# Optimization experiments

Measured on AMD Instinct MI355X. Metric: run time of the kernel, lower is better.

## Reference

```python
import jax, jax.numpy as jnp
import numpy as np

B, T, DIM, H, HD, K = 4, 2048, 1024, 16, 64, 4
QK = H * HD          # 1024
VD = 2 * H * HD      # 2048
EPS = 1e-5


def zrms(x, g):
    # zero-centered RMS norm with learned scale
    x = x - jnp.mean(x, axis=-1, keepdims=True)
    return x * jax.lax.rsqrt(jnp.mean(x * x, axis=-1, keepdims=True) + EPS) * g


def causal_dwconv(x, w):
    # x: [B,T,C], w: [K,1,C] (keras depthwise Conv1D kernel, groups=C)
    k = w.shape[0]
    return jax.lax.conv_general_dilated(
        x, w, window_strides=(1,), padding=[(k - 1, 0)],
        dimension_numbers=('NWC', 'WIO', 'NWC'),
        feature_group_count=x.shape[-1])


def setup_inputs() -> dict:
    key = jax.random.key(0)
    ks = jax.random.split(key, 12)
    s = lambda *sh: 1.0 / np.sqrt(sh[0])
    return {
        'x':  jax.random.normal(ks[0], (B, T, DIM), jnp.float32),
        'Wq': jax.random.normal(ks[1], (DIM, QK), jnp.float32) * s(DIM),
        'Wk': jax.random.normal(ks[2], (DIM, QK), jnp.float32) * s(DIM),
        'Wv': jax.random.normal(ks[3], (DIM, VD), jnp.float32) * s(DIM),
        'gq': jnp.ones((QK,), jnp.float32),
        'gk': jnp.ones((QK,), jnp.float32),
        'gv': jnp.ones((VD,), jnp.float32),
        'cq': jax.random.normal(ks[4], (K, 1, QK), jnp.float32) * 0.5,
        'ck': jax.random.normal(ks[5], (K, 1, QK), jnp.float32) * 0.5,
        'cv': jax.random.normal(ks[6], (K, 1, VD), jnp.float32) * 0.5,
        'Wa': jax.random.normal(ks[7], (DIM, H), jnp.float32) * s(DIM),
        'Wb': jax.random.normal(ks[8], (DIM, H), jnp.float32) * s(DIM),
        'Wo': jax.random.normal(ks[9], (VD, DIM), jnp.float32) * s(VD),
        'Wg': jax.random.normal(ks[10], (DIM, DIM), jnp.float32) * s(DIM),
    }


def reference(x, Wq, Wk, Wv, gq, gk, gv, cq, ck, cv, Wa, Wb, Wo, Wg):
    # 1) projections  2) zero-centered RMSNorm  3) causal depthwise conv (+silu)
    q = jax.nn.silu(causal_dwconv(zrms(x @ Wq, gq), cq))   # [B,T,QK]
    k = jax.nn.silu(causal_dwconv(zrms(x @ Wk, gk), ck))   # [B,T,QK]
    v = jax.nn.silu(causal_dwconv(zrms(x @ Wv, gv), cv))   # [B,T,VD]

    q = q.reshape(B, T, H, HD)
    k = k.reshape(B, T, H, HD)
    v = v.reshape(B, T, H, 2 * HD)

    # 4) per-head gating params
    alpha = jax.nn.sigmoid(x @ Wa)  # [B,T,H]
    beta = jax.nn.sigmoid(x @ Wb)   # [B,T,H]

    # 5) gated delta-rule recurrence over time (state S: [B,H,2*HD,HD])
    def step(S, inp):
        qt, kt, vt, at, bt = inp  # [B,H,HD],[B,H,HD],[B,H,2HD],[B,H],[B,H]
        a = at[..., None, None]
        upd = S + bt[..., None, None] * jnp.einsum('bhv,bhk->bhvk', vt, kt)
        S = a * upd + (1.0 - a) * S
        o = jnp.einsum('bhvk,bhk->bhv', S, qt)  # Q_t readout
        return S, o

    S0 = jnp.zeros((B, H, 2 * HD, HD), x.dtype)
    xs = (q.transpose(1, 0, 2, 3), k.transpose(1, 0, 2, 3),
          v.transpose(1, 0, 2, 3), alpha.transpose(1, 0, 2),
          beta.transpose(1, 0, 2))
    _, o = jax.lax.scan(step, S0, xs)          # o: [T,B,H,2HD]
    o = o.transpose(1, 0, 2, 3).reshape(B, T, VD)

    # 6) output projection + sigmoid output gate
    proj = o @ Wo                              # [B,T,DIM]
    return jax.nn.sigmoid(proj @ Wg) * proj
```

## Files before the change

kernel.cpp:

```cpp
#include <hip/hip_runtime.h>
#include <hip/hip_bf16.h>
#include <math.h>

#define RTOT 8192
#define TSEQ 2048

typedef __attribute__((ext_vector_type(8))) short short8;
typedef __attribute__((ext_vector_type(4))) float f32x4;
typedef unsigned short u16;
typedef unsigned int u32;

union U16x8 { uint4 v; u16 s[8]; };

__device__ __forceinline__ float sigmoidf_(float x) { return 1.f / (1.f + expf(-x)); }
__device__ __forceinline__ float bf2f(u16 v) { u32 u = ((u32)v) << 16; float f; __builtin_memcpy(&f, &u, 4); return f; }
__device__ __forceinline__ u16 f2bf(float f) {
  u32 u; __builtin_memcpy(&u, &f, 4);
  u32 r = (u + 0x7FFFu + ((u >> 16) & 1u)) >> 16;
  return (u16)r;
}
__device__ __forceinline__ void split2(float x, u16& h, u16& l) {
  u16 hh = f2bf(x);
  float hf = bf2f(hh);
  h = hh; l = f2bf(x - hf);
}

typedef const void __attribute__((address_space(1))) gvoid_t;
typedef void __attribute__((address_space(3))) lvoid_t;
__device__ __forceinline__ void gload_lds16(const void* g, void* l) {
  __builtin_amdgcn_global_load_lds((gvoid_t*)g, (lvoid_t*)l, 16, 0, 0);
}

__device__ __forceinline__ void xcd_remap(int& bx, int& by) {
  int gx = gridDim.x, nwg = gx * gridDim.y;
  int bid = blockIdx.y * gx + blockIdx.x;
  int cpx = nwg >> 3;
  int swz = (bid & 7) * cpx + (bid >> 3);
  bx = swz % gx; by = swz / gx;
}

__global__ __launch_bounds__(512) void gemm_sp_big(const u16* __restrict__ Ah, const u16* __restrict__ Al,
                                                   const u16* __restrict__ Bh, const u16* __restrict__ Bl,
                                                   float* __restrict__ Cf,
                                                   int M, int N, int K) {
  __shared__ u16 lds[2][4][256 * 32];
  int bx, by; xcd_remap(bx, by);
  const int tid = threadIdx.x;
  const int l = tid & 63, w = tid >> 6;
  const int wr = w >> 2, wc = w & 3;
  const int m0 = by * 256, n0 = bx * 256;
  const int fr = l & 15, fq = l >> 4;
  const int koff = 8 * (fq ^ (fr & 3));
  const int srow = tid >> 2;
  const int scol = ((tid & 3) ^ (srow & 3)) * 8;
  const u16* gA_h = Ah + (size_t)(m0 + srow) * K + scol;
  const u16* gA_l = Al + (size_t)(m0 + srow) * K + scol;
  const u16* gB_h = Bh + (size_t)(n0 + srow) * K + scol;
  const u16* gB_l = Bl + (size_t)(n0 + srow) * K + scol;
  const int lo = srow * 32 + (tid & 3) * 8;
  const int NT = K >> 5;

#define STG(buf, mat, src, t)                                 \
  do {                                                        \
    const int k0_ = (t) << 5;                                 \
    gload_lds16(src + k0_, &lds[buf][mat][lo]);               \
    gload_lds16(src + 128 * K + k0_, &lds[buf][mat][lo + 4096]); \
  } while (0)

#define MFMA_PAIR(mi, a_h, a_l)                                                        \
  do {                                                                                 \
    _Pragma("unroll")                                                                  \
    for (int n = 0; n < 4; ++n) {                                                      \
      acc[mi][n] = __builtin_amdgcn_mfma_f32_16x16x32_bf16(a_h, bh8[n], acc[mi][n], 0, 0, 0); \
      acc[mi][n] = __builtin_amdgcn_mfma_f32_16x16x32_bf16(a_h, bl8[n], acc[mi][n], 0, 0, 0); \
      acc[mi][n] = __builtin_amdgcn_mfma_f32_16x16x32_bf16(a_l, bh8[n], acc[mi][n], 0, 0, 0); \
    }                                                                                  \
  } while (0)

  f32x4 acc[8][4] = {};
  STG(0, 0, gA_h, 0); STG(0, 1, gA_l, 0); STG(0, 2, gB_h, 0); STG(0, 3, gB_l, 0);
  asm volatile("s_waitcnt vmcnt(0)" ::: "memory");
  __builtin_amdgcn_s_barrier();

  for (int t = 0; t < NT; ++t) {
    const int c = t & 1, o = c ^ 1;
    const bool pf = (t + 1 < NT);
    short8 bh8[4], bl8[4];
    {
#pragma unroll
      for (int n = 0; n < 4; ++n) {
        bh8[n] = *(const short8*)&lds[c][2][(wc * 64 + n * 16 + fr) * 32 + koff];
        bl8[n] = *(const short8*)&lds[c][3][(wc * 64 + n * 16 + fr) * 32 + koff];
      }
      short8 a0h = *(const short8*)&lds[c][0][(wr * 128 + 0 * 16 + fr) * 32 + koff];
      short8 a1h = *(const short8*)&lds[c][0][(wr * 128 + 1 * 16 + fr) * 32 + koff];
      short8 a0l = *(const short8*)&lds[c][1][(wr * 128 + 0 * 16 + fr) * 32 + koff];
      short8 a1l = *(const short8*)&lds[c][1][(wr * 128 + 1 * 16 + fr) * 32 + koff];
      if (pf) { STG(o, 2, gB_h, t + 1); STG(o, 3, gB_l, t + 1); }
      __builtin_amdgcn_s_barrier();
      asm volatile("s_waitcnt lgkmcnt(0)" ::: "memory");
      __builtin_amdgcn_s_setprio(1);
      MFMA_PAIR(0, a0h, a0l);
      MFMA_PAIR(1, a1h, a1l);
      __builtin_amdgcn_s_setprio(0);
      __builtin_amdgcn_s_barrier();
    }
    {
      short8 a0h = *(const short8*)&lds[c][0][(wr * 128 + 2 * 16 + fr) * 32 + koff];
      short8 a1h = *(const short8*)&lds[c][0][(wr * 128 + 3 * 16 + fr) * 32 + koff];
      short8 a0l = *(const short8*)&lds[c][1][(wr * 128 + 2 * 16 + fr) * 32 + koff];
      short8 a1l = *(const short8*)&lds[c][1][(wr * 128 + 3 * 16 + fr) * 32 + koff];
      if (pf) { STG(o, 0, gA_h, t + 1); STG(o, 1, gA_l, t + 1); }
      __builtin_amdgcn_s_barrier();
      asm volatile("s_waitcnt lgkmcnt(0)" ::: "memory");
      __builtin_amdgcn_s_setprio(1);
      MFMA_PAIR(2, a0h, a0l);
      MFMA_PAIR(3, a1h, a1l);
      __builtin_amdgcn_s_setprio(0);
      __builtin_amdgcn_s_barrier();
    }
    {
      short8 a0h = *(const short8*)&lds[c][0][(wr * 128 + 4 * 16 + fr) * 32 + koff];
      short8 a1h = *(const short8*)&lds[c][0][(wr * 128 + 5 * 16 + fr) * 32 + koff];
      short8 a0l = *(const short8*)&lds[c][1][(wr * 128 + 4 * 16 + fr) * 32 + koff];
      short8 a1l = *(const short8*)&lds[c][1][(wr * 128 + 5 * 16 + fr) * 32 + koff];
      __builtin_amdgcn_s_barrier();
      asm volatile("s_waitcnt lgkmcnt(0)" ::: "memory");
      __builtin_amdgcn_s_setprio(1);
      MFMA_PAIR(4, a0h, a0l);
      MFMA_PAIR(5, a1h, a1l);
      __builtin_amdgcn_s_setprio(0);
      __builtin_amdgcn_s_barrier();
    }
    {
      short8 a0h = *(const short8*)&lds[c][0][(wr * 128 + 6 * 16 + fr) * 32 + koff];
      short8 a1h = *(const short8*)&lds[c][0][(wr * 128 + 7 * 16 + fr) * 32 + koff];
      short8 a0l = *(const short8*)&lds[c][1][(wr * 128 + 6 * 16 + fr) * 32 + koff];
      short8 a1l = *(const short8*)&lds[c][1][(wr * 128 + 7 * 16 + fr) * 32 + koff];
      __builtin_amdgcn_s_barrier();
      asm volatile("s_waitcnt lgkmcnt(0)" ::: "memory");
      __builtin_amdgcn_s_setprio(1);
      MFMA_PAIR(6, a0h, a0l);
      MFMA_PAIR(7, a1h, a1l);
      __builtin_amdgcn_s_setprio(0);
      if (pf) asm volatile("s_waitcnt vmcnt(0)" ::: "memory");
      __builtin_amdgcn_s_barrier();
    }
  }
#undef STG
#undef MFMA_PAIR
#pragma unroll
  for (int m = 0; m < 8; ++m)
#pragma unroll
    for (int n = 0; n < 4; ++n)
#pragma unroll
      for (int r = 0; r < 4; ++r)
        Cf[(size_t)(m0 + wr * 128 + m * 16 + 4 * fq + r) * N + (n0 + wc * 64 + n * 16 + fr)] = acc[m][n][r];
}

template<int EPI>
__global__ __launch_bounds__(256) void gemm_sp(const u16* __restrict__ Ah, const u16* __restrict__ Al,
                                               const u16* __restrict__ Bh, const u16* __restrict__ Bl,
                                               float* __restrict__ Cf, u16* __restrict__ Ph,
                                               u16* __restrict__ Pl, const u16* __restrict__ Pinh,
                                               const u16* __restrict__ Pinl,
                                               int M, int N, int K) {
  __shared__ u16 Ash[128 * 32], Asl[128 * 32];
  __shared__ u16 Bsh[128 * 32], Bsl[128 * 32];
  int bx, by; xcd_remap(bx, by);
  const int tid = threadIdx.x;
  const int l = tid & 63, w = tid >> 6;
  const int m0 = by * 128, n0 = bx * 128;
  const int wr = w >> 1, wc = w & 1;
  f32x4 acc[4][4] = {};
  const int srow = (w << 5) + (l >> 2);
  const int scol = (l & 3) << 3;
  const size_t gA = (size_t)(m0 + srow) * K + scol;
  const size_t gB = (size_t)(n0 + srow) * K + scol;
  const int lo0 = (w * 2 + 0) * 512, lo1 = (w * 2 + 1) * 512;
  const int arow = wr * 64 + (l & 15), brow = wc * 64 + (l & 15);
  const int koff = 8 * (l >> 4);
  for (int k0 = 0; k0 < K; k0 += 32) {
    gload_lds16(Ah + gA + k0, &Ash[lo0]);
    gload_lds16(Ah + gA + 16 * K + k0, &Ash[lo1]);
    gload_lds16(Al + gA + k0, &Asl[lo0]);
    gload_lds16(Al + gA + 16 * K + k0, &Asl[lo1]);
    gload_lds16(Bh + gB + k0, &Bsh[lo0]);
    gload_lds16(Bh + gB + 16 * K + k0, &Bsh[lo1]);
    gload_lds16(Bl + gB + k0, &Bsl[lo0]);
    gload_lds16(Bl + gB + 16 * K + k0, &Bsl[lo1]);
    __syncthreads();
    short8 afh[4], afl[4], bfh[4], bfl[4];
#pragma unroll
    for (int m = 0; m < 4; ++m) {
      afh[m] = *(const short8*)&Ash[(arow + m * 16) * 32 + koff];
      afl[m] = *(const short8*)&Asl[(arow + m * 16) * 32 + koff];
    }
#pragma unroll
    for (int n = 0; n < 4; ++n) {
      bfh[n] = *(const short8*)&Bsh[(brow + n * 16) * 32 + koff];
      bfl[n] = *(const short8*)&Bsl[(brow + n * 16) * 32 + koff];
    }
#pragma unroll
    for (int m = 0; m < 4; ++m)
#pragma unroll
      for (int n = 0; n < 4; ++n) {
        acc[m][n] = __builtin_amdgcn_mfma_f32_16x16x32_bf16(afh[m], bfh[n], acc[m][n], 0, 0, 0);
        acc[m][n] = __builtin_amdgcn_mfma_f32_16x16x32_bf16(afh[m], bfl[n], acc[m][n], 0, 0, 0);
        acc[m][n] = __builtin_amdgcn_mfma_f32_16x16x32_bf16(afl[m], bfh[n], acc[m][n], 0, 0, 0);
      }
    __syncthreads();
  }
  const int rbase = m0 + wr * 64 + 4 * (l >> 4);
  const int cbase = n0 + wc * 64 + (l & 15);
#pragma unroll
  for (int m = 0; m < 4; ++m)
#pragma unroll
    for (int n = 0; n < 4; ++n)
#pragma unroll
      for (int r = 0; r < 4; ++r) {
        size_t idx = (size_t)(rbase + m * 16 + r) * N + (cbase + n * 16);
        float v = acc[m][n][r];
        if (EPI == 0) {
          Cf[idx] = v;
        } else if (EPI == 1) {
          u16 h, lo; split2(v, h, lo);
          Ph[idx] = h; Pl[idx] = lo;
        } else {
          float pin = bf2f(Pinh[idx]) + bf2f(Pinl[idx]);
          Cf[idx] = pin * sigmoidf_(v);
        }
      }
}

__global__ __launch_bounds__(256) void transcast_sp(const float* __restrict__ W,
                                                    u16* __restrict__ Wth, u16* __restrict__ Wtl,
                                                    int K, int N) {
  __shared__ float t[32][33];
  const int n0 = blockIdx.x * 32, k0 = blockIdx.y * 32;
  const int c = threadIdx.x & 31, rq = threadIdx.x >> 5;
#pragma unroll
  for (int i = 0; i < 4; ++i) t[rq * 4 + i][c] = W[(size_t)(k0 + rq * 4 + i) * N + n0 + c];
  __syncthreads();
#pragma unroll
  for (int i = 0; i < 4; ++i) {
    float v = t[c][rq * 4 + i];
    u16 h, lo; split2(v, h, lo);
    size_t idx = (size_t)(n0 + rq * 4 + i) * K + k0 + c;
    Wth[idx] = h; Wtl[idx] = lo;
  }
}

__global__ __launch_bounds__(256) void castx_sp(const float* __restrict__ x,
                                                u16* __restrict__ xh, u16* __restrict__ xl) {
  size_t i = (size_t)blockIdx.x * 256 + threadIdx.x;
  float4 v = ((const float4*)x)[i];
  ushort4 hh, ll;
  split2(v.x, hh.x, ll.x); split2(v.y, hh.y, ll.y);
  split2(v.z, hh.z, ll.z); split2(v.w, hh.w, ll.w);
  ((ushort4*)xh)[i] = hh; ((ushort4*)xl)[i] = ll;
}

template<int C, int GSCALE>
__global__ __launch_bounds__(C / 4) void conv_fs(const float* __restrict__ zn,
                                                 const float* __restrict__ w,
                                                 const float* __restrict__ g,
                                                 const float* __restrict__ gab,
                                                 u16* __restrict__ oh,
                                                 u16* __restrict__ ol) {
  constexpr int NW = C / 256;
  __shared__ float redA[NW * 4];
  __shared__ float redB[NW * 4];
  const int tid = threadIdx.x;
  const int row = blockIdx.x;
  const int t = row & (TSEQ - 1);
  const int c = tid * 4;
  const int lane = tid & 63, wid = tid >> 6;
  float4 xv[4];
  float psum[4];
#pragma unroll
  for (int d = 0; d < 4; ++d) {
    if (t - d >= 0) xv[d] = *(const float4*)(zn + (size_t)(row - d) * 4096 + c);
    else { xv[d].x = 0.f; xv[d].y = 0.f; xv[d].z = 0.f; xv[d].w = 0.f; }
    psum[d] = xv[d].x + xv[d].y + xv[d].z + xv[d].w;
  }
#pragma unroll
  for (int d = 0; d < 4; ++d)
#pragma unroll
    for (int o = 32; o > 0; o >>= 1) psum[d] += __shfl_xor(psum[d], o, 64);
  if (lane == 0) {
    redA[wid * 4 + 0] = psum[0]; redA[wid * 4 + 1] = psum[1];
    redA[wid * 4 + 2] = psum[2]; redA[wid * 4 + 3] = psum[3];
  }
  __syncthreads();
  float mean[4];
#pragma unroll
  for (int d = 0; d < 4; ++d) {
    float s = 0.f;
#pragma unroll
    for (int j = 0; j < NW; ++j) s += redA[j * 4 + d];
    mean[d] = s * (1.f / C);
  }
  float psq[4];
#pragma unroll
  for (int d = 0; d < 4; ++d) {
    float a = xv[d].x - mean[d], b = xv[d].y - mean[d];
    float e = xv[d].z - mean[d], f = xv[d].w - mean[d];
    psq[d] = a * a + b * b + e * e + f * f;
  }
#pragma unroll
  for (int d = 0; d < 4; ++d)
#pragma unroll
    for (int o = 32; o > 0; o >>= 1) psq[d] += __shfl_xor(psq[d], o, 64);
  if (lane == 0) {
    redB[wid * 4 + 0] = psq[0]; redB[wid * 4 + 1] = psq[1];
    redB[wid * 4 + 2] = psq[2]; redB[wid * 4 + 3] = psq[3];
  }
  __syncthreads();
  float rstd[4];
#pragma unroll
  for (int d = 0; d < 4; ++d) {
    float s = 0.f;
#pragma unroll
    for (int j = 0; j < NW; ++j) s += redB[j * 4 + d];
    rstd[d] = rsqrtf(s * (1.f / C) + 1e-5f);
  }
  float4 g4 = *(const float4*)(g + c);
  float4 acc; acc.x = 0.f; acc.y = 0.f; acc.z = 0.f; acc.w = 0.f;
#pragma unroll
  for (int d = 0; d < 4; ++d) {
    if (t - d >= 0) {
      float4 wv = *(const float4*)(w + (size_t)(3 - d) * C + c);
      acc.x = fmaf((xv[d].x - mean[d]) * rstd[d] * g4.x, wv.x, acc.x);
      acc.y = fmaf((xv[d].y - mean[d]) * rstd[d] * g4.y, wv.y, acc.y);
      acc.z = fmaf((xv[d].z - mean[d]) * rstd[d] * g4.z, wv.z, acc.z);
      acc.w = fmaf((xv[d].w - mean[d]) * rstd[d] * g4.w, wv.w, acc.w);
    }
  }
  float a0 = acc.x * sigmoidf_(acc.x);
  float a1 = acc.y * sigmoidf_(acc.y);
  float a2 = acc.z * sigmoidf_(acc.z);
  float a3 = acc.w * sigmoidf_(acc.w);
  if (GSCALE) {
    float gv = gab[(size_t)row * 16 + (c >> 7)];
    a0 *= gv; a1 *= gv; a2 *= gv; a3 *= gv;
  }
  ushort4 hh, ll;
  split2(a0, hh.x, ll.x); split2(a1, hh.y, ll.y);
  split2(a2, hh.z, ll.z); split2(a3, hh.w, ll.w);
  *(ushort4*)(oh + (size_t)row * C + c) = hh;
  *(ushort4*)(ol + (size_t)row * C + c) = ll;
}

__global__ __launch_bounds__(256) void gab_kernel(const float* __restrict__ x,
                                                  const float* __restrict__ Wa,
                                                  const float* __restrict__ Wb,
                                                  float* __restrict__ gout) {
  __shared__ float xs[1024];
  __shared__ float partial[256];
  const int tid = threadIdx.x;
  const size_t row = blockIdx.x;
  *(float4*)(&xs[tid*4]) = *(const float4*)(x + row*1024 + tid*4);
  __syncthreads();
  const int h = tid & 31;
  const int seg = tid >> 5;
  const float* W = (h < 16) ? Wa : Wb;
  const int col = h & 15;
  float s = 0.f;
  const int k0 = seg * 128;
  for (int k = 0; k < 128; ++k) s = fmaf(xs[k0 + k], W[(size_t)(k0 + k) * 16 + col], s);
  partial[tid] = s;
  __syncthreads();
  if (tid < 32) {
    float t2 = 0.f;
#pragma unroll
    for (int j = 0; j < 8; ++j) t2 += partial[j*32 + tid];
    partial[tid] = t2;
  }
  __syncthreads();
  if (tid < 16)
    gout[row*16 + tid] = sigmoidf_(partial[tid]) * sigmoidf_(partial[tid + 16]);
}

__global__ __launch_bounds__(256) void scan_kernel(const u16* __restrict__ kh,
                                                   const u16* __restrict__ kl,
                                                   const u16* __restrict__ vgh,
                                                   const u16* __restrict__ vgl,
                                                   u16* __restrict__ Sph,
                                                   u16* __restrict__ Spl) {
  __shared__ float Ks[64][36];
  __shared__ float Vs[64][36];
  const int tid = threadIdx.x;
  const int bid = blockIdx.x;
  const int kq = bid & 1, vq = (bid >> 1) & 3, h = (bid >> 3) & 15, b = bid >> 7;
  const size_t rb = (size_t)b * TSEQ;
  const int vd_t = tid >> 3, kd0 = (tid & 7) * 4;
  float S[4] = {};
  const int sr = tid >> 2;
  const int cc0 = (tid & 3) * 8;
  for (int c = 0; c < 32; ++c) {
    {
      size_t koffg = (rb + (size_t)c * 64 + sr) * 1024 + h * 64 + kq * 32 + cc0;
      U16x8 a0, b0;
      a0.v = *(const uint4*)(kh + koffg);
      b0.v = *(const uint4*)(kl + koffg);
#pragma unroll
      for (int j = 0; j < 8; ++j) Ks[sr][cc0 + j] = bf2f(a0.s[j]) + bf2f(b0.s[j]);
      size_t voffg = (rb + (size_t)c * 64 + sr) * 2048 + h * 128 + vq * 32 + cc0;
      U16x8 va, vb;
      va.v = *(const uint4*)(vgh + voffg);
      vb.v = *(const uint4*)(vgl + voffg);
#pragma unroll
      for (int j = 0; j < 8; ++j) Vs[sr][cc0 + j] = bf2f(va.s[j]) + bf2f(vb.s[j]);
    }
    {
      size_t spc = (((size_t)(b * 16 + h) * 32) + c) * 8192
                 + (size_t)(vq * 32 + vd_t) * 64 + kq * 32 + kd0;
      ushort4 h0, l0;
      split2(S[0], h0.x, l0.x); split2(S[1], h0.y, l0.y);
      split2(S[2], h0.z, l0.z); split2(S[3], h0.w, l0.w);
      *(ushort4*)(Sph + spc) = h0;
      *(ushort4*)(Spl + spc) = l0;
    }
    __syncthreads();
    for (int s = 0; s < 64; ++s) {
      float vv = Vs[s][vd_t];
      float kv[4];
      *(float4*)kv = *(const float4*)&Ks[s][kd0];
#pragma unroll
      for (int j = 0; j < 4; ++j) S[j] = fmaf(vv, kv[j], S[j]);
    }
    __syncthreads();
  }
}

__global__ __launch_bounds__(256) void pass2_sp(const u16* __restrict__ qh,
                                                const u16* __restrict__ ql,
                                                const u16* __restrict__ kh,
                                                const u16* __restrict__ vgh,
                                                const u16* __restrict__ Sph,
                                                const u16* __restrict__ Spl,
                                                u16* __restrict__ oh,
                                                u16* __restrict__ ol) {
  __shared__ u16 Qsh[64 * 72];
  __shared__ u16 Qsl[64 * 72];
  __shared__ u16 Ksm[64 * 72];
  __shared__ u16 Am[64 * 72];
  __shared__ u16 Vth[128 * 72];
  const int tid = threadIdx.x;
  const int l = tid & 63, w = tid >> 6;
  const int bid = blockIdx.x;
  const int c = bid & 31, h = (bid >> 5) & 15, b = bid >> 9;
  const size_t rb = (size_t)b * TSEQ + c * 64;
  const int fr = l & 15, fq = l >> 4;
  {
    int r = tid >> 2, c0 = (tid & 3) * 16;
    size_t off = (rb + r) * 1024 + h * 64 + c0;
    *(uint4*)&Qsh[r * 72 + c0]     = *(const uint4*)(qh + off);
    *(uint4*)&Qsh[r * 72 + c0 + 8] = *(const uint4*)(qh + off + 8);
    *(uint4*)&Qsl[r * 72 + c0]     = *(const uint4*)(ql + off);
    *(uint4*)&Qsl[r * 72 + c0 + 8] = *(const uint4*)(ql + off + 8);
    *(uint4*)&Ksm[r * 72 + c0]     = *(const uint4*)(kh + off);
    *(uint4*)&Ksm[r * 72 + c0 + 8] = *(const uint4*)(kh + off + 8);
  }
  {
    int s = tid >> 2, vd0 = (tid & 3) * 32;
    size_t off = (rb + s) * 2048 + h * 128 + vd0;
#pragma unroll
    for (int m4 = 0; m4 < 4; ++m4) {
      U16x8 r_; r_.v = *(const uint4*)(vgh + off + m4 * 8);
#pragma unroll
      for (int j = 0; j < 8; ++j) Vth[(vd0 + m4 * 8 + j) * 72 + s] = r_.s[j];
    }
  }
  __syncthreads();
  short8 aqh[2], aql[2];
#pragma unroll
  for (int kk = 0; kk < 2; ++kk) {
    aqh[kk] = *(const short8*)&Qsh[(w * 16 + fr) * 72 + kk * 32 + 8 * fq];
    aql[kk] = *(const short8*)&Qsl[(w * 16 + fr) * 72 + kk * 32 + 8 * fq];
  }
  f32x4 accA[4] = {};
#pragma unroll
  for (int n = 0; n < 4; ++n)
#pragma unroll
    for (int kk = 0; kk < 2; ++kk) {
      short8 bk = *(const short8*)&Ksm[(n * 16 + fr) * 72 + kk * 32 + 8 * fq];
      accA[n] = __builtin_amdgcn_mfma_f32_16x16x32_bf16(aqh[kk], bk, accA[n], 0, 0, 0);
    }
#pragma unroll
  for (int n = 0; n < 4; ++n)
#pragma unroll
    for (int rr = 0; rr < 4; ++rr) {
      int tt = w * 16 + 4 * fq + rr;
      int s = n * 16 + fr;
      Am[tt * 72 + s] = f2bf((s <= tt) ? accA[n][rr] : 0.f);
    }
  __syncthreads();
  f32x4 acc[8] = {};
#pragma unroll
  for (int kk = 0; kk < 2; ++kk) {
    short8 aa = *(const short8*)&Am[(w * 16 + fr) * 72 + kk * 32 + 8 * fq];
#pragma unroll
    for (int n = 0; n < 8; ++n) {
      short8 bv = *(const short8*)&Vth[(n * 16 + fr) * 72 + kk * 32 + 8 * fq];
      acc[n] = __builtin_amdgcn_mfma_f32_16x16x32_bf16(aa, bv, acc[n], 0, 0, 0);
    }
  }
  const size_t spb = (((size_t)(b * 16 + h) * 32) + c) * 8192;
#pragma unroll
  for (int n = 0; n < 8; ++n)
#pragma unroll
    for (int kk = 0; kk < 2; ++kk) {
      size_t soff = spb + (size_t)(n * 16 + fr) * 64 + kk * 32 + 8 * fq;
      short8 bh_ = *(const short8*)(Sph + soff);
      short8 bl_ = *(const short8*)(Spl + soff);
      acc[n] = __builtin_amdgcn_mfma_f32_16x16x32_bf16(aqh[kk], bh_, acc[n], 0, 0, 0);
      acc[n] = __builtin_amdgcn_mfma_f32_16x16x32_bf16(aqh[kk], bl_, acc[n], 0, 0, 0);
      acc[n] = __builtin_amdgcn_mfma_f32_16x16x32_bf16(aql[kk], bh_, acc[n], 0, 0, 0);
    }
#pragma unroll
  for (int n = 0; n < 8; ++n)
#pragma unroll
    for (int rr = 0; rr < 4; ++rr) {
      int tt = w * 16 + 4 * fq + rr;
      int vd = n * 16 + fr;
      u16 hh, ll;
      split2(acc[n][rr], hh, ll);
      size_t off = (rb + tt) * 2048 + h * 128 + vd;
      oh[off] = hh; ol[off] = ll;
    }
}

extern "C" void kernel_launch(void* const* d_in, const int* in_sizes, int n_in,
                              void* d_out, int out_size, void* d_ws, size_t ws_size,
                              hipStream_t stream) {
  (void)in_sizes; (void)n_in; (void)out_size; (void)ws_size;
  const float* x  = (const float*)d_in[0];
  const float* Wq = (const float*)d_in[1];
  const float* Wk = (const float*)d_in[2];
  const float* Wv = (const float*)d_in[3];
  const float* gq = (const float*)d_in[4];
  const float* gk = (const float*)d_in[5];
  const float* gv = (const float*)d_in[6];
  const float* cq = (const float*)d_in[7];
  const float* ck = (const float*)d_in[8];
  const float* cv = (const float*)d_in[9];
  const float* Wa = (const float*)d_in[10];
  const float* Wb = (const float*)d_in[11];
  const float* Wo = (const float*)d_in[12];
  const float* Wg = (const float*)d_in[13];
  float* out = (float*)d_out;
  char* ws = (char*)d_ws;

  const size_t MiB = 1024 * 1024;
  u16* Wqkv_h = (u16*)(ws + 0 * MiB);
  u16* Wqkv_l = (u16*)(ws + 8 * MiB);
  u16* Wo_h   = (u16*)(ws + 16 * MiB);
  u16* Wo_l   = (u16*)(ws + 20 * MiB);
  u16* Wg_h   = (u16*)(ws + 24 * MiB);
  u16* Wg_l   = (u16*)(ws + 26 * MiB);
  float* gbuf = (float*)(ws + 28 * MiB);
  u16* x_h    = (u16*)(ws + 32 * MiB);
  u16* x_l    = (u16*)(ws + 48 * MiB);
  float* qkv  = (float*)(ws + 64 * MiB);
  u16* q_h = (u16*)(ws + 192 * MiB);
  u16* q_l = (u16*)(ws + 208 * MiB);
  u16* k_h = (u16*)(ws + 224 * MiB);
  u16* k_l = (u16*)(ws + 240 * MiB);
  u16* vg_h = (u16*)(ws + 32 * MiB);
  u16* vg_l = (u16*)d_out;
  u16* Sp_h = (u16*)(ws + 96 * MiB);
  u16* Sp_l = (u16*)(ws + 128 * MiB);
  u16* o_h  = (u16*)(ws + 64 * MiB);
  u16* o_l  = (u16*)d_out;
  u16* p_h  = (u16*)(ws + 96 * MiB);
  u16* p_l  = (u16*)(ws + 112 * MiB);

  dim3 blk(256);
  castx_sp<<<dim3(8192), blk, 0, stream>>>(x, x_h, x_l);
  transcast_sp<<<dim3(32, 32), blk, 0, stream>>>(Wq, Wqkv_h, Wqkv_l, 1024, 1024);
  transcast_sp<<<dim3(32, 32), blk, 0, stream>>>(Wk, Wqkv_h + 1024 * 1024, Wqkv_l + 1024 * 1024, 1024, 1024);
  transcast_sp<<<dim3(64, 32), blk, 0, stream>>>(Wv, Wqkv_h + 2048 * 1024, Wqkv_l + 2048 * 1024, 1024, 2048);
  transcast_sp<<<dim3(32, 64), blk, 0, stream>>>(Wo, Wo_h, Wo_l, 2048, 1024);
  transcast_sp<<<dim3(32, 32), blk, 0, stream>>>(Wg, Wg_h, Wg_l, 1024, 1024);
  gab_kernel<<<dim3(8192), blk, 0, stream>>>(x, Wa, Wb, gbuf);
  gemm_sp_big<<<dim3(16, 32), dim3(512), 0, stream>>>(x_h, x_l, Wqkv_h, Wqkv_l, qkv, 8192, 4096, 1024);
  conv_fs<1024, 0><<<dim3(8192), dim3(256), 0, stream>>>(qkv, cq, gq, nullptr, q_h, q_l);
  conv_fs<1024, 0><<<dim3(8192), dim3(256), 0, stream>>>(qkv + 1024, ck, gk, nullptr, k_h, k_l);
  conv_fs<2048, 1><<<dim3(8192), dim3(512), 0, stream>>>(qkv + 2048, cv, gv, gbuf, vg_h, vg_l);
  scan_kernel<<<dim3(512), blk, 0, stream>>>(k_h, k_l, vg_h, vg_l, Sp_h, Sp_l);
  pass2_sp<<<dim3(2048), blk, 0, stream>>>(q_h, q_l, k_h, vg_h, Sp_h, Sp_l, o_h, o_l);
  gemm_sp<1><<<dim3(8, 64), blk, 0, stream>>>(o_h, o_l, Wo_h, Wo_l, nullptr, p_h, p_l, nullptr, nullptr, 8192, 1024, 2048);
  gemm_sp<3><<<dim3(8, 64), blk, 0, stream>>>(p_h, p_l, Wg_h, Wg_l, out, nullptr, nullptr, p_h, p_l, 8192, 1024, 1024);
}
```

Before: 669.1 us.

## Double-buffer output GEMMs, fuse cast with gate kernel, remap conv row order

The output-projection and gate GEMMs are replaced by a 512-thread, 128x256-tile kernel. It double-buffers LDS, uses a swizzled LDS layout, prefetches the next K tile while the current MFMAs run, and raises wave priority during compute. The x split-cast and the alpha/beta gate kernel are merged into one pass over x, dropping a launch and a re-read of x. conv_fs blocks are remapped so consecutive blocks touch different batches/time regions, which changes cache locality. The larger tile halves the grid to 256 blocks, which may underfill the GPU.

```diff
diff --git a/kernel.cpp b/kernel.cpp
--- a/kernel.cpp
+++ b/kernel.cpp
@@ -159,60 +159,102 @@
 }
 
 template<int EPI>
-__global__ __launch_bounds__(256) void gemm_sp(const u16* __restrict__ Ah, const u16* __restrict__ Al,
-                                               const u16* __restrict__ Bh, const u16* __restrict__ Bl,
-                                               float* __restrict__ Cf, u16* __restrict__ Ph,
-                                               u16* __restrict__ Pl, const u16* __restrict__ Pinh,
-                                               const u16* __restrict__ Pinl,
-                                               int M, int N, int K) {
-  __shared__ u16 Ash[128 * 32], Asl[128 * 32];
-  __shared__ u16 Bsh[128 * 32], Bsl[128 * 32];
+__global__ __launch_bounds__(512) void gemm_sp_mid(const u16* __restrict__ Ah, const u16* __restrict__ Al,
+                                                   const u16* __restrict__ Bh, const u16* __restrict__ Bl,
+                                                   float* __restrict__ Cf, u16* __restrict__ Ph,
+                                                   u16* __restrict__ Pl, const u16* __restrict__ Pinh,
+                                                   const u16* __restrict__ Pinl,
+                                                   int M, int N, int K) {
+  __shared__ u16 lds[2][24576];
   int bx, by; xcd_remap(bx, by);
   const int tid = threadIdx.x;
   const int l = tid & 63, w = tid >> 6;
-  const int m0 = by * 128, n0 = bx * 128;
-  const int wr = w >> 1, wc = w & 1;
+  const int wr = w >> 2, wc = w & 3;
+  const int m0 = by * 128, n0 = bx * 256;
+  const int fr = l & 15, fq = l >> 4;
+  const int koff = 8 * (fq ^ (fr & 3));
+  const int srow = tid >> 2;
+  const int scol = ((tid & 3) ^ (srow & 3)) * 8;
+  const u16* gA_h = Ah + (size_t)(m0 + srow) * K + scol;
+  const u16* gA_l = Al + (size_t)(m0 + srow) * K + scol;
+  const u16* gB_h = Bh + (size_t)(n0 + srow) * K + scol;
+  const u16* gB_l = Bl + (size_t)(n0 + srow) * K + scol;
+  const int lo = srow * 32 + (tid & 3) * 8;
+  const int NT = K >> 5;
+
+#define STGA(buf, t)                                              \
+  do {                                                            \
+    const int k0_ = (t) << 5;                                     \
+    gload_lds16(gA_h + k0_, &lds[buf][lo]);                       \
+    gload_lds16(gA_l + k0_, &lds[buf][4096 + lo]);                \
+  } while (0)
+#define STGB(buf, t)                                              \
+  do {                                                            \
+    const int k0_ = (t) << 5;                                     \
+    gload_lds16(gB_h + k0_, &lds[buf][8192 + lo]);                \
+    gload_lds16(gB_h + 128 * K + k0_, &lds[buf][8192 + 4096 + lo]); \
+    gload_lds16(gB_l + k0_, &lds[buf][16384 + lo]);               \
+    gload_lds16(gB_l + 128 * K + k0_, &lds[buf][16384 + 4096 + lo]); \
+  } while (0)
+#define MFMA_PAIR(mi, a_h, a_l)                                                        \
+  do {                                                                                 \
+    _Pragma("unroll")                                                                  \
+    for (int n = 0; n < 4; ++n) {                                                      \
+      acc[mi][n] = __builtin_amdgcn_mfma_f32_16x16x32_bf16(a_h, bh8[n], acc[mi][n], 0, 0, 0); \
+      acc[mi][n] = __builtin_amdgcn_mfma_f32_16x16x32_bf16(a_h, bl8[n], acc[mi][n], 0, 0, 0); \
+      acc[mi][n] = __builtin_amdgcn_mfma_f32_16x16x32_bf16(a_l, bh8[n], acc[mi][n], 0, 0, 0); \
+    }                                                                                  \
+  } while (0)
+
   f32x4 acc[4][4] = {};
-  const int srow = (w << 5) + (l >> 2);
-  const int scol = (l & 3) << 3;
-  const size_t gA = (size_t)(m0 + srow) * K + scol;
-  const size_t gB = (size_t)(n0 + srow) * K + scol;
-  const int lo0 = (w * 2 + 0) * 512, lo1 = (w * 2 + 1) * 512;
-  const int arow = wr * 64 + (l & 15), brow = wc * 64 + (l & 15);
-  const int koff = 8 * (l >> 4);
-  for (int k0 = 0; k0 < K; k0 += 32) {
-    gload_lds16(Ah + gA + k0, &Ash[lo0]);
-    gload_lds16(Ah + gA + 16 * K + k0, &Ash[lo1]);
-    gload_lds16(Al + gA + k0, &Asl[lo0]);
-    gload_lds16(Al + gA + 16 * K + k0, &Asl[lo1]);
-    gload_lds16(Bh + gB + k0, &Bsh[lo0]);
-    gload_lds16(Bh + gB + 16 * K + k0, &Bsh[lo1]);
-    gload_lds16(Bl + gB + k0, &Bsl[lo0]);
-    gload_lds16(Bl + gB + 16 * K + k0, &Bsl[lo1]);
-    __syncthreads();
-    short8 afh[4], afl[4], bfh[4], bfl[4];
-#pragma unroll
-    for (int m = 0; m < 4; ++m) {
-      afh[m] = *(const short8*)&Ash[(arow + m * 16) * 32 + koff];
-      afl[m] = *(const short8*)&Asl[(arow + m * 16) * 32 + koff];
-    }
-#pragma unroll
-    for (int n = 0; n < 4; ++n) {
-      bfh[n] = *(const short8*)&Bsh[(brow + n * 16) * 32 + koff];
-      bfl[n] = *(const short8*)&Bsl[(brow + n * 16) * 32 + koff];
-    }
-#pragma unroll
-    for (int m = 0; m < 4; ++m)
+  STGA(0, 0); STGB(0, 0);
+  asm volatile("s_waitcnt vmcnt(0)" ::: "memory");
+  __builtin_amdgcn_s_barrier();
+
+  for (int t = 0; t < NT; ++t) {
+    const int c = t & 1, o = c ^ 1;
+    const bool pf = (t + 1 < NT);
+    short8 bh8[4], bl8[4];
+    {
 #pragma unroll
       for (int n = 0; n < 4; ++n) {
-        acc[m][n] = __builtin_amdgcn_mfma_f32_16x16x32_bf16(afh[m], bfh[n], acc[m][n], 0, 0, 0);
-        acc[m][n] = __builtin_amdgcn_mfma_f32_16x16x32_bf16(afh[m], bfl[n], acc[m][n], 0, 0, 0);
-        acc[m][n] = __builtin_amdgcn_mfma_f32_16x16x32_bf16(afl[m], bfh[n], acc[m][n], 0, 0, 0);
+        bh8[n] = *(const short8*)&lds[c][8192 + (wc * 64 + n * 16 + fr) * 32 + koff];
+        bl8[n] = *(const short8*)&lds[c][16384 + (wc * 64 + n * 16 + fr) * 32 + koff];
       }
-    __syncthreads();
-  }
-  const int rbase = m0 + wr * 64 + 4 * (l >> 4);
-  const int cbase = n0 + wc * 64 + (l & 15);
+      short8 a0h = *(const short8*)&lds[c][(wr * 64 + 0 * 16 + fr) * 32 + koff];
+      short8 a1h = *(const short8*)&lds[c][(wr * 64 + 1 * 16 + fr) * 32 + koff];
+      short8 a0l = *(const short8*)&lds[c][4096 + (wr * 64 + 0 * 16 + fr) * 32 + koff];
+      short8 a1l = *(const short8*)&lds[c][4096 + (wr * 64 + 1 * 16 + fr) * 32 + koff];
+      if (pf) STGB(o, t + 1);
+      __builtin_amdgcn_s_barrier();
+      asm volatile("s_waitcnt lgkmcnt(0)" ::: "memory");
+      __builtin_amdgcn_s_setprio(1);
+      MFMA_PAIR(0, a0h, a0l);
+      MFMA_PAIR(1, a1h, a1l);
+      __builtin_amdgcn_s_setprio(0);
+      __builtin_amdgcn_s_barrier();
+    }
+    {
+      short8 a0h = *(const short8*)&lds[c][(wr * 64 + 2 * 16 + fr) * 32 + koff];
+      short8 a1h = *(const short8*)&lds[c][(wr * 64 + 3 * 16 + fr) * 32 + koff];
+      short8 a0l = *(const short8*)&lds[c][4096 + (wr * 64 + 2 * 16 + fr) * 32 + koff];
+      short8 a1l = *(const short8*)&lds[c][4096 + (wr * 64 + 3 * 16 + fr) * 32 + koff];
+      if (pf) STGA(o, t + 1);
+      __builtin_amdgcn_s_barrier();
+      asm volatile("s_waitcnt lgkmcnt(0)" ::: "memory");
+      __builtin_amdgcn_s_setprio(1);
+      MFMA_PAIR(2, a0h, a0l);
+      MFMA_PAIR(3, a1h, a1l);
+      __builtin_amdgcn_s_setprio(0);
+      if (pf) asm volatile("s_waitcnt vmcnt(0)" ::: "memory");
+      __builtin_amdgcn_s_barrier();
+    }
+  }
+#undef STGA
+#undef STGB
+#undef MFMA_PAIR
+  const int rbase = m0 + wr * 64 + 4 * fq;
+  const int cbase = n0 + wc * 64 + fr;
 #pragma unroll
   for (int m = 0; m < 4; ++m)
 #pragma unroll
@@ -221,11 +263,9 @@
       for (int r = 0; r < 4; ++r) {
         size_t idx = (size_t)(rbase + m * 16 + r) * N + (cbase + n * 16);
         float v = acc[m][n][r];
-        if (EPI == 0) {
-          Cf[idx] = v;
-        } else if (EPI == 1) {
-          u16 h, lo; split2(v, h, lo);
-          Ph[idx] = h; Pl[idx] = lo;
+        if (EPI == 1) {
+          u16 h, lo2; split2(v, h, lo2);
+          Ph[idx] = h; Pl[idx] = lo2;
         } else {
           float pin = bf2f(Pinh[idx]) + bf2f(Pinl[idx]);
           Cf[idx] = pin * sigmoidf_(v);
@@ -251,14 +291,41 @@
   }
 }
 
-__global__ __launch_bounds__(256) void castx_sp(const float* __restrict__ x,
-                                                u16* __restrict__ xh, u16* __restrict__ xl) {
-  size_t i = (size_t)blockIdx.x * 256 + threadIdx.x;
-  float4 v = ((const float4*)x)[i];
+__global__ __launch_bounds__(256) void castx_gab(const float* __restrict__ x,
+                                                 u16* __restrict__ xh, u16* __restrict__ xl,
+                                                 const float* __restrict__ Wa,
+                                                 const float* __restrict__ Wb,
+                                                 float* __restrict__ gout) {
+  __shared__ float xs[1024];
+  __shared__ float partial[256];
+  const int tid = threadIdx.x;
+  const size_t row = blockIdx.x;
+  float4 v = *(const float4*)(x + row * 1024 + tid * 4);
+  *(float4*)(&xs[tid * 4]) = v;
   ushort4 hh, ll;
   split2(v.x, hh.x, ll.x); split2(v.y, hh.y, ll.y);
   split2(v.z, hh.z, ll.z); split2(v.w, hh.w, ll.w);
-  ((ushort4*)xh)[i] = hh; ((ushort4*)xl)[i] = ll;
+  *(ushort4*)(xh + row * 1024 + tid * 4) = hh;
+  *(ushort4*)(xl + row * 1024 + tid * 4) = ll;
+  __syncthreads();
+  const int h = tid & 31;
+  const int seg = tid >> 5;
+  const float* W = (h < 16) ? Wa : Wb;
+  const int col = h & 15;
+  float s = 0.f;
+  const int k0 = seg * 128;
+  for (int k = 0; k < 128; ++k) s = fmaf(xs[k0 + k], W[(size_t)(k0 + k) * 16 + col], s);
+  partial[tid] = s;
+  __syncthreads();
+  if (tid < 32) {
+    float t2 = 0.f;
+#pragma unroll
+    for (int j = 0; j < 8; ++j) t2 += partial[j * 32 + tid];
+    partial[tid] = t2;
+  }
+  __syncthreads();
+  if (tid < 16)
+    gout[row * 16 + tid] = sigmoidf_(partial[tid]) * sigmoidf_(partial[tid + 16]);
 }
 
 template<int C, int GSCALE>
@@ -272,7 +339,8 @@
   __shared__ float redA[NW * 4];
   __shared__ float redB[NW * 4];
   const int tid = threadIdx.x;
-  const int row = blockIdx.x;
+  const int bid = blockIdx.x;
+  const int row = ((bid & 7) << 10) + (bid >> 3);
   const int t = row & (TSEQ - 1);
   const int c = tid * 4;
   const int lane = tid & 63, wid = tid >> 6;
@@ -350,36 +418,6 @@
   split2(a2, hh.z, ll.z); split2(a3, hh.w, ll.w);
   *(ushort4*)(oh + (size_t)row * C + c) = hh;
   *(ushort4*)(ol + (size_t)row * C + c) = ll;
-}
-
-__global__ __launch_bounds__(256) void gab_kernel(const float* __restrict__ x,
-                                                  const float* __restrict__ Wa,
-                                                  const float* __restrict__ Wb,
-                                                  float* __restrict__ gout) {
-  __shared__ float xs[1024];
-  __shared__ float partial[256];
-  const int tid = threadIdx.x;
-  const size_t row = blockIdx.x;
-  *(float4*)(&xs[tid*4]) = *(const float4*)(x + row*1024 + tid*4);
-  __syncthreads();
-  const int h = tid & 31;
-  const int seg = tid >> 5;
-  const float* W = (h < 16) ? Wa : Wb;
-  const int col = h & 15;
-  float s = 0.f;
-  const int k0 = seg * 128;
-  for (int k = 0; k < 128; ++k) s = fmaf(xs[k0 + k], W[(size_t)(k0 + k) * 16 + col], s);
-  partial[tid] = s;
-  __syncthreads();
-  if (tid < 32) {
-    float t2 = 0.f;
-#pragma unroll
-    for (int j = 0; j < 8; ++j) t2 += partial[j*32 + tid];
-    partial[tid] = t2;
-  }
-  __syncthreads();
-  if (tid < 16)
-    gout[row*16 + tid] = sigmoidf_(partial[tid]) * sigmoidf_(partial[tid + 16]);
 }
 
 __global__ __launch_bounds__(256) void scan_kernel(const u16* __restrict__ kh,
@@ -578,19 +616,18 @@
   u16* p_l  = (u16*)(ws + 112 * MiB);
 
   dim3 blk(256);
-  castx_sp<<<dim3(8192), blk, 0, stream>>>(x, x_h, x_l);
+  castx_gab<<<dim3(8192), blk, 0, stream>>>(x, x_h, x_l, Wa, Wb, gbuf);
   transcast_sp<<<dim3(32, 32), blk, 0, stream>>>(Wq, Wqkv_h, Wqkv_l, 1024, 1024);
   transcast_sp<<<dim3(32, 32), blk, 0, stream>>>(Wk, Wqkv_h + 1024 * 1024, Wqkv_l + 1024 * 1024, 1024, 1024);
   transcast_sp<<<dim3(64, 32), blk, 0, stream>>>(Wv, Wqkv_h + 2048 * 1024, Wqkv_l + 2048 * 1024, 1024, 2048);
   transcast_sp<<<dim3(32, 64), blk, 0, stream>>>(Wo, Wo_h, Wo_l, 2048, 1024);
   transcast_sp<<<dim3(32, 32), blk, 0, stream>>>(Wg, Wg_h, Wg_l, 1024, 1024);
-  gab_kernel<<<dim3(8192), blk, 0, stream>>>(x, Wa, Wb, gbuf);
   gemm_sp_big<<<dim3(16, 32), dim3(512), 0, stream>>>(x_h, x_l, Wqkv_h, Wqkv_l, qkv, 8192, 4096, 1024);
   conv_fs<1024, 0><<<dim3(8192), dim3(256), 0, stream>>>(qkv, cq, gq, nullptr, q_h, q_l);
   conv_fs<1024, 0><<<dim3(8192), dim3(256), 0, stream>>>(qkv + 1024, ck, gk, nullptr, k_h, k_l);
   conv_fs<2048, 1><<<dim3(8192), dim3(512), 0, stream>>>(qkv + 2048, cv, gv, gbuf, vg_h, vg_l);
   scan_kernel<<<dim3(512), blk, 0, stream>>>(k_h, k_l, vg_h, vg_l, Sp_h, Sp_l);
   pass2_sp<<<dim3(2048), blk, 0, stream>>>(q_h, q_l, k_h, vg_h, Sp_h, Sp_l, o_h, o_l);
-  gemm_sp<1><<<dim3(8, 64), blk, 0, stream>>>(o_h, o_l, Wo_h, Wo_l, nullptr, p_h, p_l, nullptr, nullptr, 8192, 1024, 2048);
-  gemm_sp<3><<<dim3(8, 64), blk, 0, stream>>>(p_h, p_l, Wg_h, Wg_l, out, nullptr, nullptr, p_h, p_l, 8192, 1024, 1024);
-}
+  gemm_sp_mid<1><<<dim3(4, 64), dim3(512), 0, stream>>>(o_h, o_l, Wo_h, Wo_l, nullptr, p_h, p_l, nullptr, nullptr, 8192, 1024, 2048);
+  gemm_sp_mid<3><<<dim3(4, 64), dim3(512), 0, stream>>>(p_h, p_l, Wg_h, Wg_l, out, nullptr, nullptr, p_h, p_l, 8192, 1024, 1024);
+}
```

New measurement: 665.7 us. Within noise of the previous version (-0.5%).
